# Optimization experiments

Measured on AMD Instinct MI355X. Metric: run time of the kernel, lower is better.

Reference implementation:

```python
import jax, jax.numpy as jnp
import numpy as np
from jax import lax

CHANNELS = 64
STRIDE = (2, 2, 2)
PAD = ((1, 1), (1, 1), (1, 1))  # zero pad, filt_size=3 -> pad 1 each side per spatial dim


def make_blur_filter(channels: int) -> jnp.ndarray:
    # binomial filter for filt_size=3: [1,2,1]; 3D separable outer product, normalized
    a = np.array([1.0, 2.0, 1.0], dtype=np.float32)
    f = a[:, None, None] * a[None, :, None] * a[None, None, :]
    f = f / f.sum()
    # depthwise conv kernel, OIDHW with O=channels, I=1
    return jnp.asarray(np.broadcast_to(f[None, None], (channels, 1, 3, 3, 3)).copy())


def setup_inputs() -> dict:
    key = jax.random.key(0)
    x = jax.random.normal(key, (2, CHANNELS, 64, 96, 96), dtype=jnp.float32)
    filt = make_blur_filter(CHANNELS)
    return {"x": x, "filt": filt}


def reference(x, filt):
    # zero-pad + depthwise (grouped) 3D conv with stride 2, matching
    # F.conv3d(pad(inp), filt, stride=2, groups=C)
    return lax.conv_general_dilated(
        x, filt,
        window_strides=STRIDE,
        padding=PAD,
        dimension_numbers=("NCDHW", "OIDHW", "NCDHW"),
        feature_group_count=x.shape[1],
    )
```

## Files before the change

kernel.cpp:

```cpp
#include <hip/hip_runtime.h>


namespace {
constexpr int D = 64, H = 96, W = 96;
constexpr int OD = 32, OH = 48, OW = 48;
constexpr int HW = H * W;
constexpr int YB = 16;
constexpr int ZCH = 8;
}

typedef float f4 __attribute__((ext_vector_type(4)));

__global__ __launch_bounds__(192) void blurpool3d_kernel(
    const float* __restrict__ in, float* __restrict__ out)
{
    const int xg = threadIdx.x;
    const int yl = threadIdx.y;
    const int y  = blockIdx.x * YB + yl;
    const int z0 = blockIdx.y * ZCH;
    const long nc = blockIdx.z;

    const float* __restrict__ inp = in + nc * (long)(D * HW);
    float* __restrict__ outp = out + nc * (long)(OD * OH * OW)
                                   + (long)y * OW + xg * 4;

    const int xb = xg * 8;
    const int yb = 2 * y - 1;
    const int r0i = (y > 0) ? yb : 0;
    const float w0 = (y > 0) ? 1.0f : 0.0f;
    const int r1i = yb + 1, r2i = yb + 2;
    const bool has_left = (xg > 0);

    auto rowconv = [&](const float* plane, int row) -> f4 {
        const float* r = plane + row * W + xb;
        f4 A = *(const f4*)(r);
        f4 B = *(const f4*)(r + 4);
        float h0 = has_left ? r[-1] : 0.0f;
        f4 b;
        b.x = h0  + 2.0f * A.x + A.y;
        b.y = A.y + 2.0f * A.z + A.w;
        b.z = A.w + 2.0f * B.x + B.y;
        b.w = B.y + 2.0f * B.z + B.w;
        return b;
    };

    auto planeconv = [&](const float* plane) -> f4 {
        f4 ra = rowconv(plane, r0i);
        f4 rb = rowconv(plane, r1i);
        f4 rc = rowconv(plane, r2i);
        return w0 * ra + 2.0f * rb + rc;
    };

    f4 a = {0.0f, 0.0f, 0.0f, 0.0f};
    if (z0 != 0) a = planeconv(inp + (2 * z0 - 1) * HW);

    for (int zi = 0; zi < ZCH; ++zi) {
        const int z = z0 + zi;
        f4 b = planeconv(inp + (2 * z) * HW);
        f4 c = planeconv(inp + (2 * z + 1) * HW);
        f4 o = (a + 2.0f * b + c) * 0.015625f;
        *(f4*)(outp + (long)z * (OH * OW)) = o;
        a = c;
    }
}

extern "C" void kernel_launch(void* const* d_in, const int* in_sizes, int n_in,
                              void* d_out, int out_size, void* d_ws, size_t ws_size,
                              hipStream_t stream)
{
    const float* x = (const float*)d_in[0];
    float* out = (float*)d_out;
    dim3 grid(OH / YB, OD / ZCH, 128);
    dim3 block(12, YB);
    blurpool3d_kernel<<<grid, block, 0, stream>>>(x, out);
}
```

Measured before the change: 409.5 us.

## Stage input planes through double-buffered LDS with register prefetch

Each block now cooperatively loads the 33-row slab of each input depth plane into shared memory, with a padded row pitch, and reads its 3-row windows from LDS. Before this, neighbouring threads re-read overlapping rows straight from global memory. The next plane is prefetched into registers while the current one is convolved, with double buffering and one barrier per plane. The aim is to remove redundant global and cache traffic and overlap loads with compute, at the cost of a barrier per plane, scalar LDS stores and extra shared-memory use that may lower occupancy.

```diff
diff --git a/kernel.cpp b/kernel.cpp
--- a/kernel.cpp
+++ b/kernel.cpp
@@ -7,60 +7,118 @@
 constexpr int HW = H * W;
 constexpr int YB = 16;
 constexpr int ZCH = 8;
+constexpr int NT  = 192;
+constexpr int RP  = 97;
+constexpr int MAXR = 33;
+constexpr int WF4 = W / 4;
 }
 
 typedef float f4 __attribute__((ext_vector_type(4)));
 
-__global__ __launch_bounds__(192) void blurpool3d_kernel(
+__global__ __launch_bounds__(NT) void blurpool3d_kernel(
     const float* __restrict__ in, float* __restrict__ out)
 {
-    const int xg = threadIdx.x;
-    const int yl = threadIdx.y;
-    const int y  = blockIdx.x * YB + yl;
-    const int z0 = blockIdx.y * ZCH;
+    __shared__ float lds[2][MAXR * RP];
+
+    const int xg  = threadIdx.x;
+    const int yl  = threadIdx.y;
+    const int tid = yl * 12 + xg;
+    const int y   = blockIdx.x * YB + yl;
+    const int z0  = blockIdx.y * ZCH;
     const long nc = blockIdx.z;
 
     const float* __restrict__ inp = in + nc * (long)(D * HW);
     float* __restrict__ outp = out + nc * (long)(OD * OH * OW)
                                    + (long)y * OW + xg * 4;
 
-    const int xb = xg * 8;
-    const int yb = 2 * y - 1;
-    const int r0i = (y > 0) ? yb : 0;
+    const int s0  = (blockIdx.x == 0) ? 0 : (2 * blockIdx.x * YB - 1);
+    const int nr  = (blockIdx.x == 0) ? 32 : 33;
+    const int nf4 = nr * WF4;
+
+    const int kFirst = (z0 > 0) ? (2 * z0 - 1) : 0;
+    const int nPl    = (z0 > 0) ? (2 * ZCH + 1) : (2 * ZCH);
+    const float* srcBase = inp + (long)kFirst * HW + s0 * W;
+
+    const int   yb = 2 * y - 1;
+    const int   r0 = (yb > 0 ? yb : 0) - s0;
+    const int   r1 = yb + 1 - s0;
+    const int   r2 = yb + 2 - s0;
     const float w0 = (y > 0) ? 1.0f : 0.0f;
-    const int r1i = yb + 1, r2i = yb + 2;
-    const bool has_left = (xg > 0);
+    const int   xb = xg * 8;
+    const bool  hasL = (xg > 0);
 
-    auto rowconv = [&](const float* plane, int row) -> f4 {
-        const float* r = plane + row * W + xb;
-        f4 A = *(const f4*)(r);
-        f4 B = *(const f4*)(r + 4);
-        float h0 = has_left ? r[-1] : 0.0f;
+    auto rowconvL = [&](const float* base, int row) -> f4 {
+        const float* r = base + row * RP + xb;
+        float h0 = hasL ? r[-1] : 0.0f;
+        float a0 = r[0], a1 = r[1], a2 = r[2], a3 = r[3];
+        float a4 = r[4], a5 = r[5], a6 = r[6], a7 = r[7];
         f4 b;
-        b.x = h0  + 2.0f * A.x + A.y;
-        b.y = A.y + 2.0f * A.z + A.w;
-        b.z = A.w + 2.0f * B.x + B.y;
-        b.w = B.y + 2.0f * B.z + B.w;
+        b.x = h0 + 2.0f * a0 + a1;
+        b.y = a1 + 2.0f * a2 + a3;
+        b.z = a3 + 2.0f * a4 + a5;
+        b.w = a5 + 2.0f * a6 + a7;
         return b;
     };
 
-    auto planeconv = [&](const float* plane) -> f4 {
-        f4 ra = rowconv(plane, r0i);
-        f4 rb = rowconv(plane, r1i);
-        f4 rc = rowconv(plane, r2i);
+    auto planeconvL = [&](const float* base) -> f4 {
+        f4 ra = rowconvL(base, r0);
+        f4 rb = rowconvL(base, r1);
+        f4 rc = rowconvL(base, r2);
         return w0 * ra + 2.0f * rb + rc;
     };
 
+    auto stageLoad = [&](int pk, f4* regs) {
+        const float* src = srcBase + (long)pk * HW;
+        #pragma unroll
+        for (int j = 0; j < 5; ++j) {
+            const int i = tid + j * NT;
+            if (i < nf4) regs[j] = *(const f4*)(src + 4 * i);
+        }
+    };
+    auto stageWrite = [&](float* dst, const f4* regs) {
+        #pragma unroll
+        for (int j = 0; j < 5; ++j) {
+            const int i = tid + j * NT;
+            if (i < nf4) {
+                const int row = i / WF4;
+                const int q   = i - row * WF4;
+                float* p = dst + row * RP + 4 * q;
+                p[0] = regs[j].x; p[1] = regs[j].y;
+                p[2] = regs[j].z; p[3] = regs[j].w;
+            }
+        }
+    };
+
+    f4 regs[5];
+    stageLoad(0, regs);
+    stageWrite(&lds[0][0], regs);
+    __syncthreads();
+
     f4 a = {0.0f, 0.0f, 0.0f, 0.0f};
-    if (z0 != 0) a = planeconv(inp + (2 * z0 - 1) * HW);
+    f4 b = a;
+    int buf = 0;
+    const int tOff = (z0 > 0) ? 1 : 0;
 
-    for (int zi = 0; zi < ZCH; ++zi) {
-        const int z = z0 + zi;
-        f4 b = planeconv(inp + (2 * z) * HW);
-        f4 c = planeconv(inp + (2 * z + 1) * HW);
-        f4 o = (a + 2.0f * b + c) * 0.015625f;
-        *(f4*)(outp + (long)z * (OH * OW)) = o;
-        a = c;
+    for (int k = 0; k < nPl; ++k) {
+        const bool more = (k + 1 < nPl);
+        if (more) stageLoad(k + 1, regs);
+
+        const f4 v = planeconvL(&lds[buf][0]);
+
+        const int t = k - tOff;
+        if (t < 0) {
+            a = v;
+        } else if ((t & 1) == 0) {
+            b = v;
+        } else {
+            f4 o = (a + 2.0f * b + v) * 0.015625f;
+            *(f4*)(outp + (long)(z0 + (t >> 1)) * (OH * OW)) = o;
+            a = v;
+        }
+
+        if (more) stageWrite(&lds[buf ^ 1][0], regs);
+        __syncthreads();
+        buf ^= 1;
     }
 }
 
@@ -69,8 +127,8 @@
                               hipStream_t stream)
 {
     const float* x = (const float*)d_in[0];
-    float* out = (float*)d_out;
+    float* outp = (float*)d_out;
     dim3 grid(OH / YB, OD / ZCH, 128);
     dim3 block(12, YB);
-    blurpool3d_kernel<<<grid, block, 0, stream>>>(x, out);
+    blurpool3d_kernel<<<grid, block, 0, stream>>>(x, outp);
 }
```

Result: slower. 422.1 us (+3.1%).
